# Kernel optimization log

Measured on AMD Instinct MI355X. Metric: run time of the kernel, lower is better.

## Reference

```python
import jax, jax.numpy as jnp
import numpy as np

N_NODES = 100000
N_EDGES = 1600000
IN_CH, HID_CH, OUT_CH = 128, 64, 32


def setup_inputs() -> dict:
    key = jax.random.key(0)
    k0, k1, k2, k3 = jax.random.split(key, 4)
    x = jax.random.normal(k0, (N_NODES, IN_CH), dtype=jnp.float32)
    edge_index = jax.random.randint(k1, (2, N_EDGES), 0, N_NODES, dtype=jnp.int64)
    # Glorot-style scaling for the two GCNConv weight matrices
    W1 = jax.random.normal(k2, (IN_CH, HID_CH), dtype=jnp.float32) * (2.0 / (IN_CH + HID_CH)) ** 0.5
    b1 = jnp.zeros((HID_CH,), dtype=jnp.float32)
    W2 = jax.random.normal(k3, (HID_CH, OUT_CH), dtype=jnp.float32) * (2.0 / (HID_CH + OUT_CH)) ** 0.5
    b2 = jnp.zeros((OUT_CH,), dtype=jnp.float32)
    return {"x": x, "edge_index": edge_index, "W1": W1, "b1": b1, "W2": W2, "b2": b2}


def _gcn_norm(edge_index, num_nodes):
    """Add self-loops and compute symmetric normalization deg^{-1/2}[src]*deg^{-1/2}[dst]."""
    loops = jnp.arange(num_nodes, dtype=edge_index.dtype)
    src = jnp.concatenate([edge_index[0], loops])  # message sources
    dst = jnp.concatenate([edge_index[1], loops])  # message targets
    deg = jax.ops.segment_sum(jnp.ones_like(dst, dtype=jnp.float32), dst,
                              num_segments=num_nodes)
    dinv = jnp.where(deg > 0, jax.lax.rsqrt(deg), 0.0)
    norm = dinv[src] * dinv[dst]  # [E + N]
    return src, dst, norm


def _gcn_conv(x, W, b, src, dst, norm, num_nodes):
    h = x @ W                                   # linear transform first
    msg = h[src] * norm[:, None]                # gather + scale per edge
    out = jax.ops.segment_sum(msg, dst, num_segments=num_nodes)  # scatter-add
    return out + b


def reference(x, edge_index, W1, b1, W2, b2):
    n = x.shape[0]
    src, dst, norm = _gcn_norm(edge_index, n)
    h = _gcn_conv(x, W1, b1, src, dst, norm, n)
    h = jax.nn.relu(h)
    # dropout is identity in eval mode (training=False)
    out = _gcn_conv(h, W2, b2, src, dst, norm, n)
    return out
```

## Files before the change

kernel.cpp:

```cpp
#include <hip/hip_runtime.h>

constexpr int N  = 100000;
constexpr int E  = 1600000;
constexpr int IN = 128, HID = 64, OUTC = 32;

constexpr int SHIFT = 9;
constexpr int NPB   = 1 << SHIFT;
constexpr int NB    = (N + NPB - 1) / NPB;
constexpr int CAP   = 16384;
constexpr int PB    = 256;
constexpr int CHUNK = E / PB;
constexpr int HB    = 256;

__device__ __forceinline__ unsigned short f2bf(float f) {
    union { float f; unsigned int u; } v; v.f = f;
    unsigned int u = v.u;
    return (unsigned short)((u + 0x7fffu + ((u >> 16) & 1u)) >> 16);
}
__device__ __forceinline__ float blo(unsigned u) { return __uint_as_float(u << 16); }
__device__ __forceinline__ float bhi(unsigned u) { return __uint_as_float(u & 0xffff0000u); }

__global__ __launch_bounds__(256) void k_hist(const int* __restrict__ dst,
                                              int* __restrict__ gmat) {
    __shared__ int h[NB];
    for (int i = threadIdx.x; i < NB; i += 256) h[i] = 0;
    __syncthreads();
    const int tid = blockIdx.x * 256 + threadIdx.x, nt = HB * 256;
    for (int e = tid; e < E; e += nt) atomicAdd(&h[dst[e] >> SHIFT], 1);
    __syncthreads();
    for (int i = threadIdx.x; i < NB; i += 256)
        gmat[i * HB + blockIdx.x] = h[i];
}

__global__ void k_bscan(const int* __restrict__ gmat, int* __restrict__ base,
                        int* __restrict__ cursor) {
    __shared__ int sb[256];
    const int t = threadIdx.x;
    int v = 0;
    if (t < NB) {
        const int4* row = (const int4*)(gmat + t * HB);
        #pragma unroll 8
        for (int j = 0; j < HB / 4; ++j) {
            int4 a = row[j];
            v += (a.x + a.y) + (a.z + a.w);
        }
    }
    sb[t] = v; __syncthreads();
    for (int off = 1; off < 256; off <<= 1) {
        int x = (t >= off) ? sb[t - off] : 0;
        __syncthreads();
        sb[t] += x;
        __syncthreads();
    }
    if (t < NB) { int ex = sb[t] - v; base[t] = ex; cursor[t] = ex; }
    if (t == 0) base[NB] = E;
}

__global__ __launch_bounds__(256) void k_part(const int* __restrict__ src,
                                              const int* __restrict__ dst,
                                              int* __restrict__ cursor,
                                              unsigned* __restrict__ packed) {
    __shared__ int lh[NB], lb[NB], lc[NB];
    const int t = threadIdx.x;
    const int beg = blockIdx.x * CHUNK, end = beg + CHUNK;
    for (int i = t; i < NB; i += 256) lh[i] = 0;
    __syncthreads();
    for (int e = beg + t; e < end; e += 256) atomicAdd(&lh[dst[e] >> SHIFT], 1);
    __syncthreads();
    for (int i = t; i < NB; i += 256) {
        lb[i] = lh[i] ? atomicAdd(&cursor[i], lh[i]) : 0;
        lc[i] = 0;
    }
    __syncthreads();
    for (int e = beg + t; e < end; e += 256) {
        int d = dst[e], b = d >> SHIFT;
        int idx = atomicAdd(&lc[b], 1);
        packed[lb[b] + idx] = ((unsigned)(d & (NPB - 1)) << 17) | (unsigned)src[e];
    }
}

__global__ __launch_bounds__(512) void k_build(const int* __restrict__ bbase,
                                               unsigned* __restrict__ packed,
                                               int* __restrict__ offs,
                                               float* __restrict__ dinv) {
    __shared__ int cnt[NPB];
    __shared__ unsigned stage[CAP];
    const int t = threadIdx.x, b = blockIdx.x;
    const int base = bbase[b], cntE = bbase[b + 1] - base;
    const int node0 = b << SHIFT;
    cnt[t] = 0;
    __syncthreads();
    for (int i = t; i < cntE; i += 512) atomicAdd(&cnt[packed[base + i] >> 17], 1);
    __syncthreads();
    const int v = cnt[t];
    __syncthreads();
    for (int off = 1; off < NPB; off <<= 1) {
        int x = (t >= off) ? cnt[t - off] : 0;
        __syncthreads();
        cnt[t] += x;
        __syncthreads();
    }
    const int ex = cnt[t] - v;
    const int node = node0 + t;
    if (node < N) {
        offs[node] = base + ex;
        dinv[node] = rsqrtf((float)v + 1.0f);
    }
    if (node == N) offs[N] = E;
    __syncthreads();
    cnt[t] = ex;
    __syncthreads();
    for (int i = t; i < cntE; i += 512) {
        unsigned p = packed[base + i];
        int idx = atomicAdd(&cnt[p >> 17], 1);
        if (idx < CAP) stage[idx] = p & 0x1FFFFu;
    }
    __syncthreads();
    for (int i = t; i < cntE; i += 512)
        packed[base + i] = stage[i];
}

__global__ __launch_bounds__(256) void k_gemm1(const float* __restrict__ X,
                                               const float* __restrict__ W,
                                               const float* __restrict__ dinv,
                                               unsigned short* __restrict__ Hs) {
    constexpr int R  = 32;
    constexpr int XS = IN + 4;
    __shared__ float ws[IN * HID];
    __shared__ float xs[R * XS];
    const int t    = threadIdx.x;
    const int row0 = blockIdx.x * R;

    if (blockIdx.x == 0 && t < HID / 2)
        ((unsigned*)(Hs + (size_t)N * HID))[t] = 0u;

    for (int i = t; i < IN * HID / 4; i += 256)
        ((float4*)ws)[i] = ((const float4*)W)[i];
    for (int i = t; i < R * IN / 4; i += 256) {
        int r = i / (IN / 4), k4 = i % (IN / 4);
        *(float4*)&xs[r * XS + k4 * 4] =
            ((const float4*)(X + (size_t)(row0 + r) * IN))[k4];
    }
    __syncthreads();

    const int col0 = (t & 15) * 4;
    const int r0   = (t >> 4) * 2;
    float4 a0 = {0, 0, 0, 0}, a1 = {0, 0, 0, 0};
    for (int k = 0; k < IN; ++k) {
        float4 w = *(const float4*)&ws[k * HID + col0];
        float x0 = xs[r0 * XS + k];
        float x1 = xs[(r0 + 1) * XS + k];
        a0.x += x0 * w.x; a0.y += x0 * w.y; a0.z += x0 * w.z; a0.w += x0 * w.w;
        a1.x += x1 * w.x; a1.y += x1 * w.y; a1.z += x1 * w.z; a1.w += x1 * w.w;
    }
    const float d0 = dinv[row0 + r0];
    const float d1 = dinv[row0 + r0 + 1];
    ushort4 p0 = {f2bf(a0.x * d0), f2bf(a0.y * d0), f2bf(a0.z * d0), f2bf(a0.w * d0)};
    ushort4 p1 = {f2bf(a1.x * d1), f2bf(a1.y * d1), f2bf(a1.z * d1), f2bf(a1.w * d1)};
    *(ushort4*)(Hs + (size_t)(row0 + r0) * HID + col0)       = p0;
    *(ushort4*)(Hs + (size_t)(row0 + r0 + 1) * HID + col0)   = p1;
}

__global__ __launch_bounds__(256) void k_gather1f(const int* __restrict__ offs,
                                                  const int* __restrict__ csr,
                                                  const float* __restrict__ dinv,
                                                  const unsigned short* __restrict__ Hs,
                                                  const float* __restrict__ b1,
                                                  const float* __restrict__ W2,
                                                  unsigned* __restrict__ H2u) {
    __shared__ float w2s[HID * OUTC];
    __shared__ int   sidx[4][2][96];
    __shared__ float wrow[4][2][64];
    const int t = threadIdx.x;
    if (blockIdx.x == 0 && t < OUTC / 2) H2u[(size_t)N * 16 + t] = 0u;
    for (int i = t; i < HID * OUTC / 4; i += 256)
        ((float4*)w2s)[i] = ((const float4*)W2)[i];
    __syncthreads();

    const int wave = t >> 6, lane = t & 63, half = lane >> 5, c2 = lane & 31;
    const int nA = blockIdx.x * 8 + wave * 2;
    const int myNode = nA + half;
    const int o0 = offs[myNode], o1 = offs[myNode + 1];
    const int deg  = o1 - o0;
    const int rdeg = (deg + 7) & ~7;
    for (int i = c2; i < deg; i += 32) sidx[wave][half][i] = csr[o0 + i];
    if (c2 < rdeg - deg) sidx[wave][half][deg + c2] = N;

    const unsigned* __restrict__ Hu = (const unsigned*)Hs;
    const float dn = dinv[myNode];
    unsigned su = Hu[(size_t)myNode * 32 + c2];
    float ax0 = blo(su), ay0 = bhi(su);
    float ax1 = 0, ay1 = 0, ax2 = 0, ay2 = 0, ax3 = 0, ay3 = 0;
    float ax4 = 0, ay4 = 0, ax5 = 0, ay5 = 0, ax6 = 0, ay6 = 0, ax7 = 0, ay7 = 0;
    for (int k = 0; k < rdeg; k += 8) {
        int4 sa = *(const int4*)&sidx[wave][half][k];
        int4 sb = *(const int4*)&sidx[wave][half][k + 4];
        unsigned u0 = Hu[(size_t)sa.x * 32 + c2];
        unsigned u1 = Hu[(size_t)sa.y * 32 + c2];
        unsigned u2 = Hu[(size_t)sa.z * 32 + c2];
        unsigned u3 = Hu[(size_t)sa.w * 32 + c2];
        unsigned u4 = Hu[(size_t)sb.x * 32 + c2];
        unsigned u5 = Hu[(size_t)sb.y * 32 + c2];
        unsigned u6 = Hu[(size_t)sb.z * 32 + c2];
        unsigned u7 = Hu[(size_t)sb.w * 32 + c2];
        ax0 += blo(u0);  ay0 += bhi(u0);
        ax1 += blo(u1);  ay1 += bhi(u1);
        ax2 += blo(u2);  ay2 += bhi(u2);
        ax3 += blo(u3);  ay3 += bhi(u3);
        ax4 += blo(u4);  ay4 += bhi(u4);
        ax5 += blo(u5);  ay5 += bhi(u5);
        ax6 += blo(u6);  ay6 += bhi(u6);
        ax7 += blo(u7);  ay7 += bhi(u7);
    }
    float sx = ((ax0 + ax1) + (ax2 + ax3)) + ((ax4 + ax5) + (ax6 + ax7));
    float sy = ((ay0 + ay1) + (ay2 + ay3)) + ((ay4 + ay5) + (ay6 + ay7));
    float2 bb = *(const float2*)(b1 + 2 * c2);
    wrow[wave][half][2 * c2]     = fmaxf(sx * dn + bb.x, 0.0f);
    wrow[wave][half][2 * c2 + 1] = fmaxf(sy * dn + bb.y, 0.0f);

    float acc = 0.0f;
    #pragma unroll 16
    for (int k = 0; k < HID; ++k)
        acc += wrow[wave][half][k] * w2s[k * OUTC + c2];
    float hv = acc * dn;
    float hv1 = __shfl_down(hv, 1, 64);
    if ((c2 & 1) == 0)
        H2u[(size_t)myNode * 16 + (c2 >> 1)] =
            (unsigned)f2bf(hv) | ((unsigned)f2bf(hv1) << 16);
}

__global__ __launch_bounds__(256) void k_gather2(const int* __restrict__ offs,
                                                 const int* __restrict__ csr,
                                                 const float* __restrict__ dinv,
                                                 const unsigned* __restrict__ H2u,
                                                 const float* __restrict__ b2,
                                                 float* __restrict__ out) {
    __shared__ int sidx[4][4][96];
    const int t = threadIdx.x;
    const int wave = t >> 6, lane = t & 63, q = lane >> 4, c2 = lane & 15;
    const int n0 = blockIdx.x * 16 + wave * 4;
    const int myNode = n0 + q;
    const int o0 = offs[myNode], o1 = offs[myNode + 1];
    const int deg  = o1 - o0;
    const int rdeg = (deg + 7) & ~7;
    for (int i = c2; i < deg; i += 16) sidx[wave][q][i] = csr[o0 + i];
    if (c2 < rdeg - deg) sidx[wave][q][deg + c2] = N;

    const float dn = dinv[myNode];
    unsigned su = H2u[(size_t)myNode * 16 + c2];
    float ax0 = blo(su), ay0 = bhi(su);
    float ax1 = 0, ay1 = 0, ax2 = 0, ay2 = 0, ax3 = 0, ay3 = 0;
    float ax4 = 0, ay4 = 0, ax5 = 0, ay5 = 0, ax6 = 0, ay6 = 0, ax7 = 0, ay7 = 0;
    for (int k = 0; k < rdeg; k += 8) {
        int4 sa = *(const int4*)&sidx[wave][q][k];
        int4 sb = *(const int4*)&sidx[wave][q][k + 4];
        unsigned u0 = H2u[(size_t)sa.x * 16 + c2];
        unsigned u1 = H2u[(size_t)sa.y * 16 + c2];
        unsigned u2 = H2u[(size_t)sa.z * 16 + c2];
        unsigned u3 = H2u[(size_t)sa.w * 16 + c2];
        unsigned u4 = H2u[(size_t)sb.x * 16 + c2];
        unsigned u5 = H2u[(size_t)sb.y * 16 + c2];
        unsigned u6 = H2u[(size_t)sb.z * 16 + c2];
        unsigned u7 = H2u[(size_t)sb.w * 16 + c2];
        ax0 += blo(u0);  ay0 += bhi(u0);
        ax1 += blo(u1);  ay1 += bhi(u1);
        ax2 += blo(u2);  ay2 += bhi(u2);
        ax3 += blo(u3);  ay3 += bhi(u3);
        ax4 += blo(u4);  ay4 += bhi(u4);
        ax5 += blo(u5);  ay5 += bhi(u5);
        ax6 += blo(u6);  ay6 += bhi(u6);
        ax7 += blo(u7);  ay7 += bhi(u7);
    }
    float sx = ((ax0 + ax1) + (ax2 + ax3)) + ((ax4 + ax5) + (ax6 + ax7));
    float sy = ((ay0 + ay1) + (ay2 + ay3)) + ((ay4 + ay5) + (ay6 + ay7));
    float2 bb = *(const float2*)(b2 + 2 * c2);
    float2 r;
    r.x = sx * dn + bb.x;
    r.y = sy * dn + bb.y;
    *(float2*)(out + (size_t)myNode * OUTC + 2 * c2) = r;
}

extern "C" void kernel_launch(void* const* d_in, const int* in_sizes, int n_in,
                              void* d_out, int out_size, void* d_ws, size_t ws_size,
                              hipStream_t stream) {
    const float* x   = (const float*)d_in[0];
    const int*   ei  = (const int*)d_in[1];
    const float* W1  = (const float*)d_in[2];
    const float* b1  = (const float*)d_in[3];
    const float* W2  = (const float*)d_in[4];
    const float* b2  = (const float*)d_in[5];
    float*       out = (float*)d_out;

    const int* srcp = ei;
    const int* dstp = ei + E;

    char* ws = (char*)d_ws;
    int*            bbase  = (int*)(ws + 4096);
    int*            cursor = (int*)(ws + 8192);
    int*            offs   = (int*)(ws + 16384);
    float*          dinv   = (float*)(ws + (512u << 10));
    unsigned*       packed = (unsigned*)(ws + (1u << 20));
    unsigned short* Hs     = (unsigned short*)(ws + (8u << 20));
    unsigned*       H2u    = (unsigned*)(ws + (21u << 20));
    int*            csr    = (int*)packed;
    int*            gmat   = (int*)Hs;

    k_hist <<<HB, 256, 0, stream>>>(dstp, gmat);
    k_bscan<<<1, 256, 0, stream>>>(gmat, bbase, cursor);
    k_part <<<PB, 256, 0, stream>>>(srcp, dstp, cursor, packed);
    k_build<<<NB, 512, 0, stream>>>(bbase, packed, offs, dinv);

    k_gemm1   <<<N / 32, 256, 0, stream>>>(x, W1, dinv, Hs);
    k_gather1f<<<N / 8,  256, 0, stream>>>(offs, csr, dinv, Hs, b1, W2, H2u);
    k_gather2 <<<N / 16, 256, 0, stream>>>(offs, csr, dinv, H2u, b2, out);
}
```

Measured before the change: 239.1 us.

## Raise partition block count, vectorize GEMM inner loop, split gather1 launch

Raises the edge-partition grid from 256 to 800 blocks so each block handles a smaller chunk. Unrolls the first GEMM's k-loop by four and reads x as float4 from shared memory, which cuts the number of LDS loads. Splits the fused layer-1 gather into two launches over the two halves of the node range using a node offset. The split launch adds launch overhead without an obvious benefit. CHUNK = E/PB is 2000, so it still divides evenly.

```diff
diff --git a/kernel.cpp b/kernel.cpp
--- a/kernel.cpp
+++ b/kernel.cpp
@@ -8,7 +8,7 @@
 constexpr int NPB   = 1 << SHIFT;
 constexpr int NB    = (N + NPB - 1) / NPB;
 constexpr int CAP   = 16384;
-constexpr int PB    = 256;
+constexpr int PB    = 800;
 constexpr int CHUNK = E / PB;
 constexpr int HB    = 256;
 
@@ -146,12 +146,21 @@
     const int col0 = (t & 15) * 4;
     const int r0   = (t >> 4) * 2;
     float4 a0 = {0, 0, 0, 0}, a1 = {0, 0, 0, 0};
-    for (int k = 0; k < IN; ++k) {
-        float4 w = *(const float4*)&ws[k * HID + col0];
-        float x0 = xs[r0 * XS + k];
-        float x1 = xs[(r0 + 1) * XS + k];
-        a0.x += x0 * w.x; a0.y += x0 * w.y; a0.z += x0 * w.z; a0.w += x0 * w.w;
-        a1.x += x1 * w.x; a1.y += x1 * w.y; a1.z += x1 * w.z; a1.w += x1 * w.w;
+    for (int k = 0; k < IN; k += 4) {
+        float4 x0v = *(const float4*)&xs[r0 * XS + k];
+        float4 x1v = *(const float4*)&xs[(r0 + 1) * XS + k];
+        float4 w0 = *(const float4*)&ws[(k + 0) * HID + col0];
+        float4 w1 = *(const float4*)&ws[(k + 1) * HID + col0];
+        float4 w2 = *(const float4*)&ws[(k + 2) * HID + col0];
+        float4 w3 = *(const float4*)&ws[(k + 3) * HID + col0];
+        a0.x += x0v.x * w0.x; a0.y += x0v.x * w0.y; a0.z += x0v.x * w0.z; a0.w += x0v.x * w0.w;
+        a1.x += x1v.x * w0.x; a1.y += x1v.x * w0.y; a1.z += x1v.x * w0.z; a1.w += x1v.x * w0.w;
+        a0.x += x0v.y * w1.x; a0.y += x0v.y * w1.y; a0.z += x0v.y * w1.z; a0.w += x0v.y * w1.w;
+        a1.x += x1v.y * w1.x; a1.y += x1v.y * w1.y; a1.z += x1v.y * w1.z; a1.w += x1v.y * w1.w;
+        a0.x += x0v.z * w2.x; a0.y += x0v.z * w2.y; a0.z += x0v.z * w2.z; a0.w += x0v.z * w2.w;
+        a1.x += x1v.z * w2.x; a1.y += x1v.z * w2.y; a1.z += x1v.z * w2.z; a1.w += x1v.z * w2.w;
+        a0.x += x0v.w * w3.x; a0.y += x0v.w * w3.y; a0.z += x0v.w * w3.z; a0.w += x0v.w * w3.w;
+        a1.x += x1v.w * w3.x; a1.y += x1v.w * w3.y; a1.z += x1v.w * w3.z; a1.w += x1v.w * w3.w;
     }
     const float d0 = dinv[row0 + r0];
     const float d1 = dinv[row0 + r0 + 1];
@@ -167,18 +176,19 @@
                                                   const unsigned short* __restrict__ Hs,
                                                   const float* __restrict__ b1,
                                                   const float* __restrict__ W2,
-                                                  unsigned* __restrict__ H2u) {
+                                                  unsigned* __restrict__ H2u,
+                                                  int nodeBase) {
     __shared__ float w2s[HID * OUTC];
     __shared__ int   sidx[4][2][96];
     __shared__ float wrow[4][2][64];
     const int t = threadIdx.x;
-    if (blockIdx.x == 0 && t < OUTC / 2) H2u[(size_t)N * 16 + t] = 0u;
+    if (nodeBase == 0 && blockIdx.x == 0 && t < OUTC / 2) H2u[(size_t)N * 16 + t] = 0u;
     for (int i = t; i < HID * OUTC / 4; i += 256)
         ((float4*)w2s)[i] = ((const float4*)W2)[i];
     __syncthreads();
 
     const int wave = t >> 6, lane = t & 63, half = lane >> 5, c2 = lane & 31;
-    const int nA = blockIdx.x * 8 + wave * 2;
+    const int nA = nodeBase + blockIdx.x * 8 + wave * 2;
     const int myNode = nA + half;
     const int o0 = offs[myNode], o1 = offs[myNode + 1];
     const int deg  = o1 - o0;
@@ -311,6 +321,7 @@
     k_build<<<NB, 512, 0, stream>>>(bbase, packed, offs, dinv);
 
     k_gemm1   <<<N / 32, 256, 0, stream>>>(x, W1, dinv, Hs);
-    k_gather1f<<<N / 8,  256, 0, stream>>>(offs, csr, dinv, Hs, b1, W2, H2u);
+    k_gather1f<<<N / 16, 256, 0, stream>>>(offs, csr, dinv, Hs, b1, W2, H2u, 0);
+    k_gather1f<<<N / 16, 256, 0, stream>>>(offs, csr, dinv, Hs, b1, W2, H2u, N / 2);
     k_gather2 <<<N / 16, 256, 0, stream>>>(offs, csr, dinv, H2u, b2, out);
 }
```

New measurement: 248.2 us. 1.04x slower.
